# Kernel tuning notes

Measured on AMD Instinct MI355X. Metric: run time of the kernel, lower is better.

The kernel has to match this reference:

```python
import jax, jax.numpy as jnp
import numpy as np

B, D, T, K = 32, 64, 4096, 512
COMMITMENT_COST = 0.25


def setup_inputs() -> dict:
    key = jax.random.key(0)
    k1, k2 = jax.random.split(key)
    z = jax.random.normal(k1, (B, D, T), dtype=jnp.float32)
    # nn.Embedding init: uniform(-1/K, 1/K)
    codebook = jax.random.uniform(k2, (K, D), dtype=jnp.float32,
                                  minval=-1.0 / K, maxval=1.0 / K)
    return {"z": z, "codebook": codebook}


def reference(z, codebook):
    sg = jax.lax.stop_gradient
    zt = jnp.transpose(z, (0, 2, 1))            # [B, T, D]
    zf = zt.reshape(-1, D)                      # [N, D], N = B*T
    # squared L2 distances: ||z||^2 + ||e||^2 - 2 z.e  -> [N, K]
    dists = (jnp.sum(zf * zf, axis=1, keepdims=True)
             + jnp.sum(codebook * codebook, axis=1)
             - 2.0 * jnp.matmul(zf, codebook.T))
    idx = jnp.argmin(dists, axis=1)             # [N]
    # gather codebook rows (same math as one-hot @ codebook)
    quantized = codebook[idx].reshape(zt.shape)  # [B, T, D]
    codebook_loss = jnp.mean((sg(quantized) - zt) ** 2)
    commitment_loss = jnp.mean((quantized - sg(zt)) ** 2)
    vq_loss = codebook_loss + COMMITMENT_COST * commitment_loss
    # straight-through estimator
    quantized_st = zt + sg(quantized - zt)
    quantized_out = jnp.transpose(quantized_st, (0, 2, 1))  # [B, D, T]
    indices = idx.reshape(B, T)
    return vq_loss, quantized_out, indices
```

## Files before the change

kernel.cpp:

```cpp
#include <hip/hip_runtime.h>

#define NB 32
#define ND 64
#define NT 4096
#define NK 512
#define NGRID 1024

typedef __attribute__((ext_vector_type(8))) short short8;
typedef __attribute__((ext_vector_type(16))) float f32x16;
typedef unsigned int uint32;
typedef unsigned short ushort16_t;

#define PERM(r) ((((r) & 7) * 16) + ((r) >> 3))
#define STR 68
#define ESTR 66
#define MARGIN 4e-4f
#define RCAP 4

__device__ __forceinline__ ushort16_t bf16rne(float f) {
    uint32 u = __float_as_uint(f);
    return (ushort16_t)((u + 0x7FFFu + ((u >> 16) & 1u)) >> 16);
}
__device__ __forceinline__ float bf16tof(ushort16_t h) {
    return __uint_as_float(((uint32)h) << 16);
}

__global__ void prep_kernel(const float* __restrict__ cb,
                            uint4* __restrict__ cbfrag,
                            float* __restrict__ enorm,
                            double* __restrict__ loss_acc,
                            uint32* __restrict__ counter) {
    const int bi = blockIdx.x, tid = threadIdx.x;
    if (bi < 16) {
        const int t = bi * 256 + tid;
        const int c = t >> 8, rem = t & 255, s = rem >> 6, L = rem & 63;
        const int kcode = c * 32 + (L & 31);
        const int dbase = s * 16 + ((L >> 5) << 3);
        const float* src = cb + (size_t)kcode * 64 + dbase;
        const float4 pa = *(const float4*)src;
        const float4 pb = *(const float4*)(src + 4);
        const float f[8] = {pa.x, pa.y, pa.z, pa.w, pb.x, pb.y, pb.z, pb.w};
        uint32 hw[4], lw[4];
#pragma unroll
        for (int i = 0; i < 4; ++i) {
            const ushort16_t h0 = bf16rne(f[2*i]);
            const ushort16_t h1 = bf16rne(f[2*i+1]);
            const ushort16_t l0 = bf16rne(f[2*i]   - bf16tof(h0));
            const ushort16_t l1 = bf16rne(f[2*i+1] - bf16tof(h1));
            hw[i] = (uint32)h0 | ((uint32)h1 << 16);
            lw[i] = (uint32)l0 | ((uint32)l1 << 16);
        }
        cbfrag[(size_t)((c*4+s)*2 + 0)*64 + L] = make_uint4(hw[0],hw[1],hw[2],hw[3]);
        cbfrag[(size_t)((c*4+s)*2 + 1)*64 + L] = make_uint4(lw[0],lw[1],lw[2],lw[3]);
    } else {
        if (tid == 0) { *loss_acc = 0.0; *counter = 0u; }
        for (int k = tid; k < NK; k += 256) {
            const float* e = cb + (size_t)k * ND;
            float r[8];
#pragma unroll
            for (int j = 0; j < 8; ++j) {
                float s = __fmul_rn(e[j], e[j]);
#pragma unroll
                for (int i = 1; i < 8; ++i)
                    s = __fadd_rn(s, __fmul_rn(e[8*i+j], e[8*i+j]));
                r[j] = s;
            }
            enorm[k] = __fadd_rn(__fadd_rn(__fadd_rn(r[0],r[1]), __fadd_rn(r[2],r[3])),
                                 __fadd_rn(__fadd_rn(r[4],r[5]), __fadd_rn(r[6],r[7])));
        }
    }
}

__device__ __forceinline__ float exact_dist(const float* __restrict__ zrow,
                                            const float* __restrict__ cb,
                                            const float* __restrict__ enl,
                                            float zn, int k2) {
    const float4* e4 = (const float4*)(cb + (size_t)k2 * ND);
    float a = 0.0f;
#pragma unroll
    for (int w = 0; w < 16; ++w) {
        const float4 ev = e4[w];
        const float4 zv = *(const float4*)(zrow + 4 * w);
        a = __builtin_fmaf(zv.x, ev.x, a);
        a = __builtin_fmaf(zv.y, ev.y, a);
        a = __builtin_fmaf(zv.z, ev.z, a);
        a = __builtin_fmaf(zv.w, ev.w, a);
    }
    return __fsub_rn(__fadd_rn(zn, enl[k2]), __fmul_rn(2.0f, a));
}

__global__ __launch_bounds__(256, 3) void vq_main(const float* __restrict__ z,
                                                  const float* __restrict__ cb,
                                                  const uint4* __restrict__ cbfrag,
                                                  const float* __restrict__ enorm,
                                                  float* __restrict__ qout,
                                                  float* __restrict__ idxout,
                                                  double* __restrict__ loss_acc,
                                                  uint32* __restrict__ counter,
                                                  float* __restrict__ out0) {
    __shared__ __align__(16) char smem[46112];
    float*       zl   = (float*)smem;
    float*       enl  = (float*)(smem + 34816);
    float*       znl  = (float*)(smem + 36864);
    ushort16_t*  cand = (ushort16_t*)(smem + 37376);
    int*         sfin = (int*)(smem + 45568);
    double*      sred = (double*)(smem + 46080);

    const int bi    = blockIdx.x;
    const int b     = bi >> 5;
    const int tbase = (bi & 31) * 128;
    const int tid   = threadIdx.x;
    const size_t zoff = (size_t)b * (ND * NT) + tbase;

#pragma unroll
    for (int j = 0; j < 8; ++j) {
        const int qq = j * 256 + tid;
        const int i4 = qq & 31, d = qq >> 5;
        const float4 v = *(const float4*)(z + zoff + (size_t)d * NT + i4 * 4);
        const float vv[4] = {v.x, v.y, v.z, v.w};
#pragma unroll
        for (int c = 0; c < 4; ++c) {
            const int r = i4 * 4 + c;
            zl[PERM(r) * STR + d] = vv[c];
        }
    }
    for (int k = tid; k < NK; k += 256) enl[k] = enorm[k];
    __syncthreads();

    if (tid < 128) {
        const int r = tid;
        const float4* zr4 = (const float4*)&zl[PERM(r) * STR];
        float x[64];
#pragma unroll
        for (int wq = 0; wq < 16; ++wq) {
            const float4 t4 = zr4[wq];
            x[4*wq] = t4.x; x[4*wq+1] = t4.y; x[4*wq+2] = t4.z; x[4*wq+3] = t4.w;
        }
        float r8[8];
#pragma unroll
        for (int jj = 0; jj < 8; ++jj) {
            float s = __fmul_rn(x[jj], x[jj]);
#pragma unroll
            for (int ii = 1; ii < 8; ++ii)
                s = __fadd_rn(s, __fmul_rn(x[8*ii+jj], x[8*ii+jj]));
            r8[jj] = s;
        }
        znl[r] = __fadd_rn(__fadd_rn(__fadd_rn(r8[0],r8[1]), __fadd_rn(r8[2],r8[3])),
                           __fadd_rn(__fadd_rn(r8[4],r8[5]), __fadd_rn(r8[6],r8[7])));
    }

    const int L    = tid & 63;
    const int w    = tid >> 6;
    const int h    = L >> 5;
    const int rowl = w * 32 + (L & 31);
    short8 bhf[4], blf[4];
    {
        const float* zrow = &zl[PERM(rowl) * STR];
#pragma unroll
        for (int s = 0; s < 4; ++s) {
            const int d0 = s * 16 + h * 8;
            const float4 pa = *(const float4*)(zrow + d0);
            const float4 pb = *(const float4*)(zrow + d0 + 4);
            const float f[8] = {pa.x, pa.y, pa.z, pa.w, pb.x, pb.y, pb.z, pb.w};
            uint32 hw[4], lw[4];
#pragma unroll
            for (int i = 0; i < 4; ++i) {
                const ushort16_t h0 = bf16rne(f[2*i]);
                const ushort16_t h1 = bf16rne(f[2*i+1]);
                const ushort16_t l0 = bf16rne(f[2*i]   - bf16tof(h0));
                const ushort16_t l1 = bf16rne(f[2*i+1] - bf16tof(h1));
                hw[i] = (uint32)h0 | ((uint32)h1 << 16);
                lw[i] = (uint32)l0 | ((uint32)l1 << 16);
            }
            union { uint4 u; short8 s8; } uh, ul;
            uh.u = make_uint4(hw[0],hw[1],hw[2],hw[3]);
            ul.u = make_uint4(lw[0],lw[1],lw[2],lw[3]);
            bhf[s] = uh.s8; blf[s] = ul.s8;
        }
    }
    __syncthreads();

    float best  = __builtin_inff();
    int   bestk = 0;
    {
        uint4 buf0[8], buf1[8];
#pragma unroll
        for (int p = 0; p < 8; ++p) buf0[p] = cbfrag[(size_t)p * 64 + L];
#pragma unroll 2
        for (int c = 0; c < 16; ++c) {
            const uint4* cur = (c & 1) ? buf1 : buf0;
            uint4*       nxt = (c & 1) ? buf0 : buf1;
#pragma unroll
            for (int p = 0; p < 8; ++p)
                nxt[p] = cbfrag[(size_t)((c + 1) * 8 + p) * 64 + L];
            f32x16 acc;
#pragma unroll
            for (int r = 0; r < 16; ++r) acc[r] = 0.0f;
#pragma unroll
            for (int s = 0; s < 4; ++s) {
                union { uint4 u; short8 s8; } ah, al;
                ah.u = cur[s * 2 + 0];
                al.u = cur[s * 2 + 1];
                acc = __builtin_amdgcn_mfma_f32_32x32x16_bf16(ah.s8, bhf[s], acc, 0, 0, 0);
                acc = __builtin_amdgcn_mfma_f32_32x32x16_bf16(al.s8, bhf[s], acc, 0, 0, 0);
                acc = __builtin_amdgcn_mfma_f32_32x32x16_bf16(ah.s8, blf[s], acc, 0, 0, 0);
            }
#pragma unroll
            for (int r = 0; r < 16; ++r) {
                const int kc = c * 32 + ((r & 3) + 8 * (r >> 2) + 4 * h);
                const float sv = __builtin_fmaf(-2.0f, acc[r], enl[kc]);
                if (sv < best) { best = sv; bestk = kc; }
            }
        }
    }
    {
        const float ob  = __shfl_xor(best, 32);
        const int   obk = __shfl_xor(bestk, 32);
        if (ob < best || (ob == best && obk < bestk)) { best = ob; bestk = obk; }
    }
    const float thresh = best + MARGIN;

    int myc = 0, ovf = 0;
    ushort16_t* mylist = cand + (rowl * 2 + h) * RCAP;
    {
        uint4 buf0[8], buf1[8];
#pragma unroll
        for (int p = 0; p < 8; ++p) buf0[p] = cbfrag[(size_t)p * 64 + L];
#pragma unroll 2
        for (int c = 0; c < 16; ++c) {
            const uint4* cur = (c & 1) ? buf1 : buf0;
            uint4*       nxt = (c & 1) ? buf0 : buf1;
#pragma unroll
            for (int p = 0; p < 8; ++p)
                nxt[p] = cbfrag[(size_t)((c + 1) * 8 + p) * 64 + L];
            f32x16 acc;
#pragma unroll
            for (int r = 0; r < 16; ++r) acc[r] = 0.0f;
#pragma unroll
            for (int s = 0; s < 4; ++s) {
                union { uint4 u; short8 s8; } ah, al;
                ah.u = cur[s * 2 + 0];
                al.u = cur[s * 2 + 1];
                acc = __builtin_amdgcn_mfma_f32_32x32x16_bf16(ah.s8, bhf[s], acc, 0, 0, 0);
                acc = __builtin_amdgcn_mfma_f32_32x32x16_bf16(al.s8, bhf[s], acc, 0, 0, 0);
                acc = __builtin_amdgcn_mfma_f32_32x32x16_bf16(ah.s8, blf[s], acc, 0, 0, 0);
            }
#pragma unroll
            for (int r = 0; r < 16; ++r) {
                const int kc = c * 32 + ((r & 3) + 8 * (r >> 2) + 4 * h);
                const float sv = __builtin_fmaf(-2.0f, acc[r], enl[kc]);
                if (sv <= thresh && kc != bestk) {
                    if (myc < RCAP) mylist[myc++] = (ushort16_t)kc;
                    else ovf = 1;
                }
            }
        }
    }

    const float* zrow = &zl[PERM(rowl) * STR];
    const float  zn   = znl[rowl];
    const int    totr = myc + __shfl_xor(myc, 32);
    const int    aovf = ovf | __shfl_xor(ovf, 32);

    int bk;
    if (aovf) {
        float bd = __builtin_inff(); bk = 0x7FFFFFFF;
        for (int c = 0; c < 16; ++c)
#pragma unroll
            for (int qd = 0; qd < 4; ++qd)
#pragma unroll
                for (int i = 0; i < 4; ++i) {
                    const int k2 = c * 32 + qd * 8 + h * 4 + i;
                    const float dv = exact_dist(zrow, cb, enl, zn, k2);
                    if (dv < bd || (dv == bd && k2 < bk)) { bd = dv; bk = k2; }
                }
        const float obd = __shfl_xor(bd, 32);
        const int   obk = __shfl_xor(bk, 32);
        if (obd < bd || (obd == bd && obk < bk)) bk = obk;
    } else if (totr > 0) {
        float bd = __builtin_inff(); bk = 0x7FFFFFFF;
        if (((bestk >> 2) & 1) == h) {
            bd = exact_dist(zrow, cb, enl, zn, bestk);
            bk = bestk;
        }
        for (int i = 0; i < myc; ++i) {
            const int k2 = mylist[i];
            const float dv = exact_dist(zrow, cb, enl, zn, k2);
            if (dv < bd || (dv == bd && k2 < bk)) { bd = dv; bk = k2; }
        }
        const float obd = __shfl_xor(bd, 32);
        const int   obk = __shfl_xor(bk, 32);
        if (obd < bd || (obd == bd && obk < bk)) bk = obk;
    } else {
        bk = bestk;
    }
    if (h == 0) {
        sfin[rowl] = bk;
        idxout[(size_t)b * NT + tbase + rowl] = (float)bk;
    }
    __syncthreads();

    float* ech = zl;
#pragma unroll
    for (int j = 0; j < 8; ++j) {
        const int qq  = j * 256 + tid;
        const int row = qq >> 4, d4 = qq & 15;
        const float4 v = *(const float4*)(cb + (size_t)sfin[row] * ND + d4 * 4);
        float* dst = &ech[row * ESTR + d4 * 4];
        *(float2*)(dst)     = make_float2(v.x, v.y);
        *(float2*)(dst + 2) = make_float2(v.z, v.w);
    }
    __syncthreads();

    double lsum = 0.0;
#pragma unroll 4
    for (int j = 0; j < 32; ++j) {
        const int qq = j * 256 + tid;
        const int ir = qq & 127, d = qq >> 7;
        const float zv = z[zoff + (size_t)d * NT + ir];
        const float ev = ech[ir * ESTR + d];
        const float diff = __fsub_rn(ev, zv);
        qout[(size_t)b * (ND*NT) + (size_t)d * NT + tbase + ir] = __fadd_rn(zv, diff);
        lsum += (double)diff * (double)diff;
    }
#pragma unroll
    for (int off = 32; off > 0; off >>= 1) lsum += __shfl_down(lsum, off, 64);
    if ((tid & 63) == 0) sred[tid >> 6] = lsum;
    __syncthreads();

    if (tid == 0) {
        const double bsum = (sred[0] + sred[1]) + (sred[2] + sred[3]);
        atomicAdd(loss_acc, bsum);
        __threadfence();
        const uint32 old = atomicAdd(counter, 1u);
        if (old == (uint32)(NGRID - 1)) {
            __threadfence();
            const double tot = *(volatile double*)loss_acc;
            const double m = tot / (double)((size_t)NB * NT * ND);
            out0[0] = (float)(1.25 * m);
        }
    }
}

extern "C" void kernel_launch(void* const* d_in, const int* in_sizes, int n_in,
                              void* d_out, int out_size, void* d_ws, size_t ws_size,
                              hipStream_t stream) {
    const float* z  = (const float*)d_in[0];
    const float* cb = (const float*)d_in[1];

    float* out      = (float*)d_out;
    float* loss_out = out;
    float* qout     = out + 1;
    float* idxout   = out + 1 + (size_t)NB * ND * NT;

    uint4*  cbfrag   = (uint4*)d_ws;
    float*  enorm    = (float*)((char*)d_ws + 139264);
    double* loss_acc = (double*)((char*)d_ws + 141312);
    uint32* counter  = (uint32*)((char*)d_ws + 141320);

    prep_kernel<<<17, 256, 0, stream>>>(cb, cbfrag, enorm, loss_acc, counter);
    vq_main<<<NGRID, 256, 0, stream>>>(z, cb, cbfrag, enorm, qout, idxout,
                                       loss_acc, counter, loss_out);
}
```

Before: 200.9 us.

## Split MFMA accumulators, pack argmin keys, and raise occupancy to four blocks

The MFMA chain per 32-code chunk is split into two independent accumulators so back-to-back dependent MFMAs can overlap. The running argmin is replaced by a packed sortable uint key (truncated distance bits plus code index) reduced with a min tree instead of compare-and-branch. The candidate buffer is shrunk so shared memory and launch bounds allow four blocks per CU. Risks are extra register pressure from the second accumulator under the tighter register budget, and that the truncated distance bits coarsen the threshold, which the margin must absorb.

```diff
diff --git a/kernel.cpp b/kernel.cpp
--- a/kernel.cpp
+++ b/kernel.cpp
@@ -23,6 +23,16 @@
 }
 __device__ __forceinline__ float bf16tof(ushort16_t h) {
     return __uint_as_float(((uint32)h) << 16);
+}
+__device__ __forceinline__ uint32 encsv(float sv, int k) {
+    uint32 u = __float_as_uint(sv);
+    u = (u & 0x80000000u) ? ~u : (u | 0x80000000u);
+    return (u & 0xFFFFFE00u) | (uint32)k;
+}
+__device__ __forceinline__ float decsv(uint32 v) {
+    uint32 u = v & 0xFFFFFE00u;
+    u = (u & 0x80000000u) ? (u & 0x7FFFFFFFu) : ~u;
+    return __uint_as_float(u);
 }
 
 __global__ void prep_kernel(const float* __restrict__ cb,
@@ -89,7 +99,7 @@
     return __fsub_rn(__fadd_rn(zn, enl[k2]), __fmul_rn(2.0f, a));
 }
 
-__global__ __launch_bounds__(256, 3) void vq_main(const float* __restrict__ z,
+__global__ __launch_bounds__(256, 4) void vq_main(const float* __restrict__ z,
                                                   const float* __restrict__ cb,
                                                   const uint4* __restrict__ cbfrag,
                                                   const float* __restrict__ enorm,
@@ -98,13 +108,13 @@
                                                   double* __restrict__ loss_acc,
                                                   uint32* __restrict__ counter,
                                                   float* __restrict__ out0) {
-    __shared__ __align__(16) char smem[46112];
+    __shared__ __align__(16) char smem[39968];
     float*       zl   = (float*)smem;
     float*       enl  = (float*)(smem + 34816);
     float*       znl  = (float*)(smem + 36864);
     ushort16_t*  cand = (ushort16_t*)(smem + 37376);
-    int*         sfin = (int*)(smem + 45568);
-    double*      sred = (double*)(smem + 46080);
+    int*         sfin = (int*)(smem + 39424);
+    double*      sred = (double*)(smem + 39936);
 
     const int bi    = blockIdx.x;
     const int b     = bi >> 5;
@@ -180,8 +190,7 @@
     }
     __syncthreads();
 
-    float best  = __builtin_inff();
-    int   bestk = 0;
+    uint32 bpack = 0xFFFFFFFFu;
     {
         uint4 buf0[8], buf1[8];
 #pragma unroll
@@ -193,32 +202,45 @@
 #pragma unroll
             for (int p = 0; p < 8; ++p)
                 nxt[p] = cbfrag[(size_t)((c + 1) * 8 + p) * 64 + L];
-            f32x16 acc;
-#pragma unroll
-            for (int r = 0; r < 16; ++r) acc[r] = 0.0f;
-#pragma unroll
-            for (int s = 0; s < 4; ++s) {
+            f32x16 a0, a1;
+#pragma unroll
+            for (int r = 0; r < 16; ++r) { a0[r] = 0.0f; a1[r] = 0.0f; }
+#pragma unroll
+            for (int s = 0; s < 2; ++s) {
                 union { uint4 u; short8 s8; } ah, al;
                 ah.u = cur[s * 2 + 0];
                 al.u = cur[s * 2 + 1];
-                acc = __builtin_amdgcn_mfma_f32_32x32x16_bf16(ah.s8, bhf[s], acc, 0, 0, 0);
-                acc = __builtin_amdgcn_mfma_f32_32x32x16_bf16(al.s8, bhf[s], acc, 0, 0, 0);
-                acc = __builtin_amdgcn_mfma_f32_32x32x16_bf16(ah.s8, blf[s], acc, 0, 0, 0);
-            }
+                a0 = __builtin_amdgcn_mfma_f32_32x32x16_bf16(ah.s8, bhf[s], a0, 0, 0, 0);
+                a0 = __builtin_amdgcn_mfma_f32_32x32x16_bf16(al.s8, bhf[s], a0, 0, 0, 0);
+                a0 = __builtin_amdgcn_mfma_f32_32x32x16_bf16(ah.s8, blf[s], a0, 0, 0, 0);
+            }
+#pragma unroll
+            for (int s = 2; s < 4; ++s) {
+                union { uint4 u; short8 s8; } ah, al;
+                ah.u = cur[s * 2 + 0];
+                al.u = cur[s * 2 + 1];
+                a1 = __builtin_amdgcn_mfma_f32_32x32x16_bf16(ah.s8, bhf[s], a1, 0, 0, 0);
+                a1 = __builtin_amdgcn_mfma_f32_32x32x16_bf16(al.s8, bhf[s], a1, 0, 0, 0);
+                a1 = __builtin_amdgcn_mfma_f32_32x32x16_bf16(ah.s8, blf[s], a1, 0, 0, 0);
+            }
+            uint32 e[16];
 #pragma unroll
             for (int r = 0; r < 16; ++r) {
                 const int kc = c * 32 + ((r & 3) + 8 * (r >> 2) + 4 * h);
-                const float sv = __builtin_fmaf(-2.0f, acc[r], enl[kc]);
-                if (sv < best) { best = sv; bestk = kc; }
-            }
-        }
-    }
-    {
-        const float ob  = __shfl_xor(best, 32);
-        const int   obk = __shfl_xor(bestk, 32);
-        if (ob < best || (ob == best && obk < bestk)) { best = ob; bestk = obk; }
-    }
-    const float thresh = best + MARGIN;
+                const float sv = __builtin_fmaf(-2.0f, a0[r] + a1[r], enl[kc]);
+                e[r] = encsv(sv, kc);
+            }
+#pragma unroll
+            for (int st = 8; st > 0; st >>= 1)
+#pragma unroll
+                for (int r = 0; r < st; ++r)
+                    e[r] = min(e[r], e[r + st]);
+            bpack = min(bpack, e[0]);
+        }
+    }
+    bpack = min(bpack, (uint32)__shfl_xor((int)bpack, 32));
+    const int   bestk  = (int)(bpack & 511u);
+    const float thresh = decsv(bpack) + MARGIN;
 
     int myc = 0, ovf = 0;
     ushort16_t* mylist = cand + (rowl * 2 + h) * RCAP;
@@ -233,22 +255,31 @@
 #pragma unroll
             for (int p = 0; p < 8; ++p)
                 nxt[p] = cbfrag[(size_t)((c + 1) * 8 + p) * 64 + L];
-            f32x16 acc;
-#pragma unroll
-            for (int r = 0; r < 16; ++r) acc[r] = 0.0f;
-#pragma unroll
-            for (int s = 0; s < 4; ++s) {
+            f32x16 a0, a1;
+#pragma unroll
+            for (int r = 0; r < 16; ++r) { a0[r] = 0.0f; a1[r] = 0.0f; }
+#pragma unroll
+            for (int s = 0; s < 2; ++s) {
                 union { uint4 u; short8 s8; } ah, al;
                 ah.u = cur[s * 2 + 0];
                 al.u = cur[s * 2 + 1];
-                acc = __builtin_amdgcn_mfma_f32_32x32x16_bf16(ah.s8, bhf[s], acc, 0, 0, 0);
-                acc = __builtin_amdgcn_mfma_f32_32x32x16_bf16(al.s8, bhf[s], acc, 0, 0, 0);
-                acc = __builtin_amdgcn_mfma_f32_32x32x16_bf16(ah.s8, blf[s], acc, 0, 0, 0);
+                a0 = __builtin_amdgcn_mfma_f32_32x32x16_bf16(ah.s8, bhf[s], a0, 0, 0, 0);
+                a0 = __builtin_amdgcn_mfma_f32_32x32x16_bf16(al.s8, bhf[s], a0, 0, 0, 0);
+                a0 = __builtin_amdgcn_mfma_f32_32x32x16_bf16(ah.s8, blf[s], a0, 0, 0, 0);
+            }
+#pragma unroll
+            for (int s = 2; s < 4; ++s) {
+                union { uint4 u; short8 s8; } ah, al;
+                ah.u = cur[s * 2 + 0];
+                al.u = cur[s * 2 + 1];
+                a1 = __builtin_amdgcn_mfma_f32_32x32x16_bf16(ah.s8, bhf[s], a1, 0, 0, 0);
+                a1 = __builtin_amdgcn_mfma_f32_32x32x16_bf16(al.s8, bhf[s], a1, 0, 0, 0);
+                a1 = __builtin_amdgcn_mfma_f32_32x32x16_bf16(ah.s8, blf[s], a1, 0, 0, 0);
             }
 #pragma unroll
             for (int r = 0; r < 16; ++r) {
                 const int kc = c * 32 + ((r & 3) + 8 * (r >> 2) + 4 * h);
-                const float sv = __builtin_fmaf(-2.0f, acc[r], enl[kc]);
+                const float sv = __builtin_fmaf(-2.0f, a0[r] + a1[r], enl[kc]);
                 if (sv <= thresh && kc != bestk) {
                     if (myc < RCAP) mylist[myc++] = (ushort16_t)kc;
                     else ovf = 1;
```

Result: slower. 230.0 us (+14.5%).
